# Kernel optimization log

Hardware: AMD Instinct MI355X
Metric: run time of the kernel (lower is better)

## Reference

```python
import jax, jax.numpy as jnp
import numpy as np

NMS_KS = 15
TOP_K = 2048
GAUSS_KS = 7
GAUSS_SIGMA = 1.0
LOSS_LAMBDA = 1.0


def setup_inputs() -> dict:
    key = jax.random.key(0)
    k1, k2, k3 = jax.random.split(key, 3)
    B, H, W = 16, 1024, 1024
    score1 = jax.random.uniform(k1, (B, 1, H, W), dtype=jnp.float32)
    w_score2 = jax.random.uniform(k2, (B, 1, H, W), dtype=jnp.float32)
    w_vis_mask2 = jax.random.randint(k3, (B, 1, H, W), 0, 2) > 0
    return {"score1": score1, "w_score2": w_score2, "w_vis_mask2": w_vis_mask2}


def _nms(score, ks):
    # keep only local maxima within a ks x ks window (stride 1, 'same' padding)
    pooled = jax.lax.reduce_window(score, -jnp.inf, jax.lax.max,
                                   (1, 1, ks, ks), (1, 1, 1, 1), 'SAME')
    return jnp.where(score == pooled, score, jnp.zeros_like(score))


def _prepare_gt_score(score, nms_ks, k, mask):
    # NMS -> mask -> per-image top-k -> binary GT keypoint map
    s = _nms(score, nms_ks) * mask.astype(score.dtype)
    b = s.shape[0]
    flat = s.reshape(b, -1)                      # B x (H*W)
    _, idx = jax.lax.top_k(flat, k)              # B x k
    gt = jnp.zeros_like(flat).at[jnp.arange(b)[:, None], idx].set(1.0)
    return gt.reshape(s.shape)


def _gaussian_filter(x, ks, sigma):
    coords = jnp.arange(ks, dtype=jnp.float32) - (ks - 1) / 2.0
    g = jnp.exp(-(coords ** 2) / (2.0 * sigma ** 2))
    g = g / g.sum()
    k2d = jnp.outer(g, g)[None, None]
    pad = ks // 2
    return jax.lax.conv_general_dilated(
        x, k2d, (1, 1), [(pad, pad), (pad, pad)],
        dimension_numbers=('NCHW', 'OIHW', 'NCHW'))


def reference(score1, w_score2, w_vis_mask2):
    b = score1.shape[0]
    gt_score1 = jax.lax.stop_gradient(
        _prepare_gt_score(w_score2, NMS_KS, TOP_K, w_vis_mask2))
    gt_score1 = _gaussian_filter(gt_score1, GAUSS_KS, GAUSS_SIGMA)
    m = w_vis_mask2.astype(jnp.float32)
    loss = ((score1 - gt_score1) ** 2) * m       # masked elementwise MSE
    loss = loss.reshape(b, -1).sum(-1) / jnp.clip(m.reshape(b, -1).sum(-1), 1e-8)
    return LOSS_LAMBDA * loss.mean()
```

## Files before the change

kernel.cpp:

```cpp
#include <hip/hip_runtime.h>
#include <math.h>

#define BATCH 16
#define H 1024
#define W 1024
#define NTILES 8192
#define NBANDS (NTILES * 4)
#define CAP 4096
#define TOPK 2048
#define BCW 12

struct WS {
  float pt1[NBANDS];
  int   pmc[NBANDS];
  int   band_cnt[NBANDS];
  int   cand_count[BATCH];
  float corr_part[BATCH * 64];
  float band_val[NBANDS * BCW];
  int   band_idx[NBANDS * BCW];
  float ccand_val[BATCH * CAP];
  int   ccand_idx[BATCH * CAP];
};

__constant__ float GW[7] = {
  0.004433048175f, 0.054005582623f, 0.242036229376f, 0.399050279652f,
  0.242036229376f, 0.054005582623f, 0.004433048175f
};

__device__ __forceinline__ float4 max4(float4 a, float4 b) {
  float4 r;
  r.x = fmaxf(a.x, b.x); r.y = fmaxf(a.y, b.y);
  r.z = fmaxf(a.z, b.z); r.w = fmaxf(a.w, b.w);
  return r;
}

__global__ __launch_bounds__(256, 5) void k_nms(const float* __restrict__ score1,
                                                const float* __restrict__ score2,
                                                const int* __restrict__ mask,
                                                WS* __restrict__ ws) {
  __shared__ float4 halo[4][22][21];
  const int tid = threadIdx.x;
  const int w = tid >> 6, l = tid & 63;

  const int t = (blockIdx.x & 7) * (NTILES / 8) + (blockIdx.x >> 3);
  const int b  = t >> 9;
  const int tt = t & 511;
  const int ty0 = (tt >> 4) << 5;
  const int tx0 = (tt & 15) << 6;
  const int by0 = ty0 + (w << 3);
  const size_t ibase = (size_t)b * ((size_t)H * W);
  const float* s2 = score2 + ibase;

  const int rl = l >> 3;
  const int c8 = l & 7;
  const size_t pb = ibase + (size_t)(by0 + rl) * W + tx0 + (c8 << 3);
  const float4 s1a = *(const float4*)(score1 + pb);
  const float4 s1b = *(const float4*)(score1 + pb + 4);
  const int4  mka = *(const int4*)(mask + pb);
  const int4  mkb = *(const int4*)(mask + pb + 4);

  float4 st[7]; int sr[7], sc[7];
  #pragma unroll
  for (int k = 0; k < 7; k++) {
    const int slot = l + (k << 6);
    if (slot < 440) {
      const int r = slot / 20, c = slot - r * 20;
      sr[k] = r; sc[k] = c;
      const int gy = by0 - 7 + r, gx = tx0 - 8 + (c << 2);
      const bool ok = (gy >= 0) & (gy < H) & (gx >= 0) & (gx < W);
      const int gyc = min(max(gy, 0), H - 1);
      const int gxc = ok ? gx : 0;
      float4 v = *(const float4*)(s2 + (size_t)gyc * W + gxc);
      if (!ok) v = make_float4(-INFINITY, -INFINITY, -INFINITY, -INFINITY);
      st[k] = v;
    }
  }

  float t1 = 0.f; int mcnt = 0; unsigned int mbits = 0;
  {
    const float sc_[8] = {s1a.x, s1a.y, s1a.z, s1a.w, s1b.x, s1b.y, s1b.z, s1b.w};
    const int   mm[8] = {mka.x, mka.y, mka.z, mka.w, mkb.x, mkb.y, mkb.z, mkb.w};
    #pragma unroll
    for (int j = 0; j < 8; j++) {
      if (mm[j]) { t1 = fmaf(sc_[j], sc_[j], t1); mcnt++; mbits |= (1u << j); }
    }
  }

  #pragma unroll
  for (int k = 0; k < 7; k++) {
    const int slot = l + (k << 6);
    if (slot < 440) halo[w][sr[k]][sc[k]] = st[k];
  }
  __builtin_amdgcn_wave_barrier();
  asm volatile("s_waitcnt lgkmcnt(0)" ::: "memory");
  __builtin_amdgcn_sched_barrier(0);

  float4 vr0, vr1, vr2, vr3;
  int R0 = 0, cg = 0;
  if (l < 40) {
    const int r2 = l / 20;
    cg = l - r2 * 20;
    R0 = r2 << 2;
    float4 core = halo[w][R0 + 3][cg];
    #pragma unroll
    for (int k = 4; k <= 14; k++) core = max4(core, halo[w][R0 + k][cg]);
    const float4 h0 = halo[w][R0][cg], h1 = halo[w][R0 + 1][cg], h2 = halo[w][R0 + 2][cg];
    const float4 h15 = halo[w][R0 + 15][cg], h16 = halo[w][R0 + 16][cg], h17 = halo[w][R0 + 17][cg];
    const float4 p2 = h2, p1 = max4(h1, p2), p0 = max4(h0, p1);
    const float4 sf15 = h15, sf16 = max4(sf15, h16), sf17 = max4(sf16, h17);
    vr0 = max4(core, p0);
    vr1 = max4(max4(core, p1), sf15);
    vr2 = max4(max4(core, p2), sf16);
    vr3 = max4(core, sf17);
  }
  const float4 cva = halo[w][rl + 7][(c8 << 1) + 2];
  const float4 cvb = halo[w][rl + 7][(c8 << 1) + 3];
  __builtin_amdgcn_wave_barrier();
  asm volatile("s_waitcnt lgkmcnt(0)" ::: "memory");
  __builtin_amdgcn_sched_barrier(0);

  if (l < 40) {
    halo[w][R0 + 0][cg] = vr0;
    halo[w][R0 + 1][cg] = vr1;
    halo[w][R0 + 2][cg] = vr2;
    halo[w][R0 + 3][cg] = vr3;
  }
  __builtin_amdgcn_wave_barrier();
  asm volatile("s_waitcnt lgkmcnt(0)" ::: "memory");
  __builtin_amdgcn_sched_barrier(0);

  float r[24];
  #pragma unroll
  for (int g = 0; g < 6; g++) {
    float4 v = halo[w][rl][(c8 << 1) + g];
    r[4 * g + 0] = v.x; r[4 * g + 1] = v.y; r[4 * g + 2] = v.z; r[4 * g + 3] = v.w;
  }
  float core = r[8];
  #pragma unroll
  for (int k = 9; k <= 15; k++) core = fmaxf(core, r[k]);
  const float q7 = r[7];
  const float q6 = fmaxf(r[6], q7);
  const float q5 = fmaxf(r[5], q6);
  const float q4 = fmaxf(r[4], q5);
  const float q3 = fmaxf(r[3], q4);
  const float q2 = fmaxf(r[2], q3);
  const float q1 = fmaxf(r[1], q2);
  float sa[7];
  sa[0] = r[16];
  #pragma unroll
  for (int k = 1; k < 7; k++) sa[k] = fmaxf(sa[k - 1], r[16 + k]);
  float pooled[8];
  pooled[0] = fmaxf(core, q1);
  pooled[1] = fmaxf(fmaxf(core, q2), sa[0]);
  pooled[2] = fmaxf(fmaxf(core, q3), sa[1]);
  pooled[3] = fmaxf(fmaxf(core, q4), sa[2]);
  pooled[4] = fmaxf(fmaxf(core, q5), sa[3]);
  pooled[5] = fmaxf(fmaxf(core, q6), sa[4]);
  pooled[6] = fmaxf(fmaxf(core, q7), sa[5]);
  pooled[7] = fmaxf(core, sa[6]);

  const float cc[8] = {cva.x, cva.y, cva.z, cva.w, cvb.x, cvb.y, cvb.z, cvb.w};
  int cj = -1; float cv = 0.f;
  #pragma unroll
  for (int j = 0; j < 8; j++) {
    if (((mbits >> j) & 1u) && cj < 0) {
      const float s = cc[j];
      if (s == pooled[j] && s > 0.f) { cj = j; cv = s; }
    }
  }
  const int band = (t << 2) + w;
  const unsigned long long bal = __ballot(cj >= 0);
  if (cj >= 0) {
    const int pos = (int)__popcll(bal & ((1ull << l) - 1ull));
    if (pos < BCW) {
      ws->band_val[band * BCW + pos] = cv;
      ws->band_idx[band * BCW + pos] = (by0 + rl) * W + tx0 + (c8 << 3) + cj;
    }
  }
  #pragma unroll
  for (int off = 32; off > 0; off >>= 1) {
    t1 += __shfl_down(t1, off);
    mcnt += __shfl_down(mcnt, off);
  }
  if (l == 0) {
    int nc = (int)__popcll(bal); if (nc > BCW) nc = BCW;
    ws->band_cnt[band] = nc;
    ws->pt1[band] = t1;
    ws->pmc[band] = mcnt;
  }
}

__global__ __launch_bounds__(256) void k_compact(WS* __restrict__ ws) {
  const int b = blockIdx.x;
  const int tid = threadIdx.x;
  const int lane = tid & 63, w = tid >> 6;
  __shared__ int wt[4];

  const int base = b * 2048 + tid * 8;
  int c[8]; int csum = 0;
  #pragma unroll
  for (int u = 0; u < 8; u++) {
    int x = ws->band_cnt[base + u];
    if (x > BCW) x = BCW;
    c[u] = x; csum += x;
  }
  int v = csum;
  #pragma unroll
  for (int off = 1; off < 64; off <<= 1) {
    int u2 = __shfl_up(v, off);
    if (lane >= off) v += u2;
  }
  if (lane == 63) wt[w] = v;
  __syncthreads();
  int wo = 0;
  #pragma unroll
  for (int k = 0; k < 4; k++) if (k < w) wo += wt[k];
  const int excl = v - csum + wo;
  float* dv = ws->ccand_val + b * CAP;
  int*   di = ws->ccand_idx + b * CAP;
  if (tid == 255) {
    int tot = excl + csum;
    if (tot > CAP) tot = CAP;
    ws->cand_count[b] = tot;
    #pragma unroll
    for (int u = 0; u < 3; u++)
      if (tot + u < CAP) dv[tot + u] = 0.f;
  }
  int off = excl;
  #pragma unroll
  for (int u = 0; u < 8; u++) {
    const float* sv = ws->band_val + (size_t)(base + u) * BCW;
    const int*   si = ws->band_idx + (size_t)(base + u) * BCW;
    for (int j = 0; j < c[u]; j++) {
      if (off < CAP) { dv[off] = sv[j]; di[off] = si[j]; }
      off++;
    }
  }
}

__global__ __launch_bounds__(256, 4) void k_rankstamp(const float* __restrict__ score1,
                                                      const int* __restrict__ mask,
                                                      WS* __restrict__ ws) {
  const int blk = (blockIdx.x & 7) * 128 + (blockIdx.x >> 3);
  const int b = blk >> 6;
  const int slice = blk & 63;
  int n = ws->cand_count[b]; if (n > CAP) n = CAP;
  const int i0 = slice << 6;
  if (i0 >= n) {
    if (threadIdx.x == 0) ws->corr_part[b * 64 + slice] = 0.f;
    return;
  }
  __shared__ __align__(16) float sval[CAP];
  __shared__ __align__(16) int   sidx[CAP];
  __shared__ int   s_prank[4][64];
  __shared__ int   s_keys[64];
  __shared__ int   s_nk;
  __shared__ float cred[4];
  const int tid = threadIdx.x;
  const int w = tid >> 6, l = tid & 63;
  const int nf4 = (n + 3) >> 2;

  const float4* gv = (const float4*)(ws->ccand_val + b * CAP);
  const int4*   gi = (const int4*)(ws->ccand_idx + b * CAP);
  for (int j = tid; j < nf4; j += 256) {
    ((float4*)sval)[j] = gv[j];
    ((int4*)sidx)[j]   = gi[j];
  }
  __syncthreads();

  const float vi = sval[i0 + l];
  const int   xi = sidx[i0 + l];
  const int q = (nf4 + 3) >> 2;
  int lo = w * q; if (lo > nf4) lo = nf4;
  int hi = lo + q; if (hi > nf4) hi = nf4;
  int rank = 0;
  int j = lo;
  for (; j + 4 <= hi; j += 4) {
    #pragma unroll
    for (int u = 0; u < 4; u++) {
      const float4 vv = ((const float4*)sval)[j + u];
      const int4  iv = ((const int4*)sidx)[j + u];
      rank += (vv.x > vi) + (vv.y > vi) + (vv.z > vi) + (vv.w > vi);
      rank += (vv.x == vi && iv.x < xi);
      rank += (vv.y == vi && iv.y < xi);
      rank += (vv.z == vi && iv.z < xi);
      rank += (vv.w == vi && iv.w < xi);
    }
  }
  for (; j < hi; j++) {
    const float4 vv = ((const float4*)sval)[j];
    const int4  iv = ((const int4*)sidx)[j];
    rank += (vv.x > vi) + (vv.y > vi) + (vv.z > vi) + (vv.w > vi);
    rank += (vv.x == vi && iv.x < xi);
    rank += (vv.y == vi && iv.y < xi);
    rank += (vv.z == vi && iv.z < xi);
    rank += (vv.w == vi && iv.w < xi);
  }
  s_prank[w][l] = rank;
  __syncthreads();

  if (tid < 64) {
    const int rtot = s_prank[0][tid] + s_prank[1][tid] + s_prank[2][tid] + s_prank[3][tid];
    const bool sel = (i0 + tid < n) && (rtot < TOPK);
    const unsigned long long bal = __ballot(sel);
    if (sel) {
      const int pos = __popcll(bal & ((1ull << tid) - 1ull));
      s_keys[pos] = sidx[i0 + tid];
    }
    if (tid == 0) s_nk = (int)__popcll(bal);
  }
  __syncthreads();
  const int nk = s_nk;

  float contrib = 0.f;
  const int sub = tid & 7;
  const size_t ib2 = (size_t)b * ((size_t)H * W);
  #pragma unroll
  for (int rnd = 0; rnd < 2; rnd++) {
    const int k = (tid >> 3) + (rnd << 5);
    if (k < nk && sub < 7) {
      const int ck = s_keys[k];
      const int cy = ck >> 10, cx = ck & 1023;
      const int py = cy + sub - 3;
      const float wy = GW[sub] * ((py >= 0 && py < H) ? 1.f : 0.f);
      const int pyc = min(max(py, 0), H - 1);
      const float* s1r = score1 + ib2 + (size_t)pyc * W;
      const int*   mr  = mask   + ib2 + (size_t)pyc * W;
      #pragma unroll
      for (int dx = -3; dx <= 3; dx++) {
        const int px = cx + dx;
        const float wv = wy * GW[dx + 3] * ((px >= 0 && px < W) ? 1.f : 0.f);
        const int pxc = min(max(px, 0), W - 1);
        const float mf = (mr[pxc] != 0) ? 1.f : 0.f;
        contrib += mf * wv * (wv - 2.f * s1r[pxc]);
      }
    }
  }
  #pragma unroll
  for (int off2 = 32; off2 > 0; off2 >>= 1) contrib += __shfl_down(contrib, off2);
  if (l == 0) cred[w] = contrib;
  __syncthreads();
  if (tid == 0)
    ws->corr_part[b * 64 + slice] = (cred[0] + cred[1]) + (cred[2] + cred[3]);
}

__global__ __launch_bounds__(1024) void k_final(WS* __restrict__ ws, float* __restrict__ out) {
  const int tid = threadIdx.x;
  const int b = tid >> 6, l = tid & 63;
  __shared__ double sD[BATCH];

  double tsum = 0.0; long long msum = 0;
  const float4* pv = (const float4*)(ws->pt1 + b * 2048);
  const int4*   pm = (const int4*)(ws->pmc + b * 2048);
  #pragma unroll
  for (int k = 0; k < 8; k++) {
    const float4 f = pv[l + (k << 6)];
    const int4   m = pm[l + (k << 6)];
    tsum += (double)f.x + (double)f.y + (double)f.z + (double)f.w;
    msum += (long long)(m.x + m.y + m.z + m.w);
  }
  double csum = (double)ws->corr_part[b * 64 + l];
  #pragma unroll
  for (int off = 32; off > 0; off >>= 1) {
    tsum += __shfl_down(tsum, off);
    msum += __shfl_down(msum, off);
    csum += __shfl_down(csum, off);
  }
  if (l == 0) {
    double denom = (double)msum;
    if (denom < 1e-8) denom = 1e-8;
    sD[b] = (tsum + csum) / denom;
  }
  __syncthreads();
  if (tid == 0) {
    double acc = 0.0;
    #pragma unroll
    for (int k = 0; k < BATCH; k++) acc += sD[k];
    out[0] = (float)(acc / BATCH);
  }
}

extern "C" void kernel_launch(void* const* d_in, const int* in_sizes, int n_in,
                              void* d_out, int out_size, void* d_ws, size_t ws_size,
                              hipStream_t stream) {
  const float* score1 = (const float*)d_in[0];
  const float* score2 = (const float*)d_in[1];
  const int*   mask   = (const int*)d_in[2];
  float* out = (float*)d_out;
  WS* ws = (WS*)d_ws;

  k_nms<<<NTILES, 256, 0, stream>>>(score1, score2, mask, ws);
  k_compact<<<BATCH, 256, 0, stream>>>(ws);
  k_rankstamp<<<BATCH * 64, 256, 0, stream>>>(score1, mask, ws);
  k_final<<<1, 1024, 0, stream>>>(ws, out);
}
```

Before: 85.65 us.

## Process full 32-row tile per wave to share vertical halo across bands

Each wave now owns a whole 32x64 tile and walks its four 8-row bands in sequence, using a single 46-row shared halo instead of four separate 22-row halos. This removes the redundant 14-row vertical halo reloads between adjacent bands and reduces global score2 traffic. The second half of the halo is loaded while the first band is computed. In exchange the kernel holds more registers and LDS per wave, runs 128-thread blocks with lower occupancy, and each wave's work is serialized.

```diff
diff --git a/kernel.cpp b/kernel.cpp
--- a/kernel.cpp
+++ b/kernel.cpp
@@ -6,9 +6,16 @@
 #define W 1024
 #define NTILES 8192
 #define NBANDS (NTILES * 4)
+#define NBLK 4096
 #define CAP 4096
 #define TOPK 2048
 #define BCW 12
+
+#define SYNC_WAVE() do { \
+  __builtin_amdgcn_wave_barrier(); \
+  asm volatile("s_waitcnt lgkmcnt(0)" ::: "memory"); \
+  __builtin_amdgcn_sched_barrier(0); \
+} while (0)
 
 struct WS {
   float pt1[NBANDS];
@@ -34,160 +41,192 @@
   return r;
 }
 
-__global__ __launch_bounds__(256, 5) void k_nms(const float* __restrict__ score1,
+__global__ __launch_bounds__(128, 2) void k_nms(const float* __restrict__ score1,
                                                 const float* __restrict__ score2,
                                                 const int* __restrict__ mask,
                                                 WS* __restrict__ ws) {
-  __shared__ float4 halo[4][22][21];
+  __shared__ float4 halo[2][46][21];
   const int tid = threadIdx.x;
   const int w = tid >> 6, l = tid & 63;
 
-  const int t = (blockIdx.x & 7) * (NTILES / 8) + (blockIdx.x >> 3);
+  const int blk = (blockIdx.x & 7) * (NBLK / 8) + (blockIdx.x >> 3);
+  const int t = (blk << 1) + w;
   const int b  = t >> 9;
   const int tt = t & 511;
   const int ty0 = (tt >> 4) << 5;
   const int tx0 = (tt & 15) << 6;
-  const int by0 = ty0 + (w << 3);
   const size_t ibase = (size_t)b * ((size_t)H * W);
   const float* s2 = score2 + ibase;
-
   const int rl = l >> 3;
   const int c8 = l & 7;
-  const size_t pb = ibase + (size_t)(by0 + rl) * W + tx0 + (c8 << 3);
-  const float4 s1a = *(const float4*)(score1 + pb);
-  const float4 s1b = *(const float4*)(score1 + pb + 4);
-  const int4  mka = *(const int4*)(mask + pb);
-  const int4  mkb = *(const int4*)(mask + pb + 4);
-
-  float4 st[7]; int sr[7], sc[7];
+
+  float4 s1a[4], s1b[4]; int4 mka[4], mkb[4];
+  #pragma unroll
+  for (int k = 0; k < 4; k++) {
+    const size_t pb = ibase + (size_t)(ty0 + (k << 3) + rl) * W + tx0 + (c8 << 3);
+    s1a[k] = *(const float4*)(score1 + pb);
+    s1b[k] = *(const float4*)(score1 + pb + 4);
+    mka[k] = *(const int4*)(mask + pb);
+    mkb[k] = *(const int4*)(mask + pb + 4);
+  }
+
+  float4 stA[7]; int rA[7], cA[7];
   #pragma unroll
   for (int k = 0; k < 7; k++) {
     const int slot = l + (k << 6);
     if (slot < 440) {
       const int r = slot / 20, c = slot - r * 20;
-      sr[k] = r; sc[k] = c;
-      const int gy = by0 - 7 + r, gx = tx0 - 8 + (c << 2);
+      rA[k] = r; cA[k] = c;
+      const int gy = ty0 - 7 + r, gx = tx0 - 8 + (c << 2);
       const bool ok = (gy >= 0) & (gy < H) & (gx >= 0) & (gx < W);
       const int gyc = min(max(gy, 0), H - 1);
       const int gxc = ok ? gx : 0;
       float4 v = *(const float4*)(s2 + (size_t)gyc * W + gxc);
       if (!ok) v = make_float4(-INFINITY, -INFINITY, -INFINITY, -INFINITY);
-      st[k] = v;
-    }
-  }
-
-  float t1 = 0.f; int mcnt = 0; unsigned int mbits = 0;
-  {
-    const float sc_[8] = {s1a.x, s1a.y, s1a.z, s1a.w, s1b.x, s1b.y, s1b.z, s1b.w};
-    const int   mm[8] = {mka.x, mka.y, mka.z, mka.w, mkb.x, mkb.y, mkb.z, mkb.w};
+      stA[k] = v;
+    }
+  }
+
+  float t1[4]; int mcnt[4]; unsigned int mbits[4];
+  #pragma unroll
+  for (int k = 0; k < 4; k++) {
+    t1[k] = 0.f; mcnt[k] = 0; mbits[k] = 0;
+    const float sc_[8] = {s1a[k].x, s1a[k].y, s1a[k].z, s1a[k].w,
+                          s1b[k].x, s1b[k].y, s1b[k].z, s1b[k].w};
+    const int   mm[8] = {mka[k].x, mka[k].y, mka[k].z, mka[k].w,
+                         mkb[k].x, mkb[k].y, mkb[k].z, mkb[k].w};
     #pragma unroll
     for (int j = 0; j < 8; j++) {
-      if (mm[j]) { t1 = fmaf(sc_[j], sc_[j], t1); mcnt++; mbits |= (1u << j); }
+      if (mm[j]) { t1[k] = fmaf(sc_[j], sc_[j], t1[k]); mcnt[k]++; mbits[k] |= (1u << j); }
+    }
+  }
+
+  float4 stB[8]; int rB[8], cB[8];
+  #pragma unroll
+  for (int k = 0; k < 8; k++) {
+    const int slot = 440 + l + (k << 6);
+    if (slot < 920) {
+      const int r = slot / 20, c = slot - r * 20;
+      rB[k] = r; cB[k] = c;
+      const int gy = ty0 - 7 + r, gx = tx0 - 8 + (c << 2);
+      const bool ok = (gy >= 0) & (gy < H) & (gx >= 0) & (gx < W);
+      const int gyc = min(max(gy, 0), H - 1);
+      const int gxc = ok ? gx : 0;
+      float4 v = *(const float4*)(s2 + (size_t)gyc * W + gxc);
+      if (!ok) v = make_float4(-INFINITY, -INFINITY, -INFINITY, -INFINITY);
+      stB[k] = v;
     }
   }
 
   #pragma unroll
   for (int k = 0; k < 7; k++) {
-    const int slot = l + (k << 6);
-    if (slot < 440) halo[w][sr[k]][sc[k]] = st[k];
-  }
-  __builtin_amdgcn_wave_barrier();
-  asm volatile("s_waitcnt lgkmcnt(0)" ::: "memory");
-  __builtin_amdgcn_sched_barrier(0);
-
-  float4 vr0, vr1, vr2, vr3;
-  int R0 = 0, cg = 0;
-  if (l < 40) {
-    const int r2 = l / 20;
-    cg = l - r2 * 20;
-    R0 = r2 << 2;
-    float4 core = halo[w][R0 + 3][cg];
-    #pragma unroll
-    for (int k = 4; k <= 14; k++) core = max4(core, halo[w][R0 + k][cg]);
-    const float4 h0 = halo[w][R0][cg], h1 = halo[w][R0 + 1][cg], h2 = halo[w][R0 + 2][cg];
-    const float4 h15 = halo[w][R0 + 15][cg], h16 = halo[w][R0 + 16][cg], h17 = halo[w][R0 + 17][cg];
-    const float4 p2 = h2, p1 = max4(h1, p2), p0 = max4(h0, p1);
-    const float4 sf15 = h15, sf16 = max4(sf15, h16), sf17 = max4(sf16, h17);
-    vr0 = max4(core, p0);
-    vr1 = max4(max4(core, p1), sf15);
-    vr2 = max4(max4(core, p2), sf16);
-    vr3 = max4(core, sf17);
-  }
-  const float4 cva = halo[w][rl + 7][(c8 << 1) + 2];
-  const float4 cvb = halo[w][rl + 7][(c8 << 1) + 3];
-  __builtin_amdgcn_wave_barrier();
-  asm volatile("s_waitcnt lgkmcnt(0)" ::: "memory");
-  __builtin_amdgcn_sched_barrier(0);
-
-  if (l < 40) {
-    halo[w][R0 + 0][cg] = vr0;
-    halo[w][R0 + 1][cg] = vr1;
-    halo[w][R0 + 2][cg] = vr2;
-    halo[w][R0 + 3][cg] = vr3;
-  }
-  __builtin_amdgcn_wave_barrier();
-  asm volatile("s_waitcnt lgkmcnt(0)" ::: "memory");
-  __builtin_amdgcn_sched_barrier(0);
-
-  float r[24];
-  #pragma unroll
-  for (int g = 0; g < 6; g++) {
-    float4 v = halo[w][rl][(c8 << 1) + g];
-    r[4 * g + 0] = v.x; r[4 * g + 1] = v.y; r[4 * g + 2] = v.z; r[4 * g + 3] = v.w;
-  }
-  float core = r[8];
-  #pragma unroll
-  for (int k = 9; k <= 15; k++) core = fmaxf(core, r[k]);
-  const float q7 = r[7];
-  const float q6 = fmaxf(r[6], q7);
-  const float q5 = fmaxf(r[5], q6);
-  const float q4 = fmaxf(r[4], q5);
-  const float q3 = fmaxf(r[3], q4);
-  const float q2 = fmaxf(r[2], q3);
-  const float q1 = fmaxf(r[1], q2);
-  float sa[7];
-  sa[0] = r[16];
-  #pragma unroll
-  for (int k = 1; k < 7; k++) sa[k] = fmaxf(sa[k - 1], r[16 + k]);
-  float pooled[8];
-  pooled[0] = fmaxf(core, q1);
-  pooled[1] = fmaxf(fmaxf(core, q2), sa[0]);
-  pooled[2] = fmaxf(fmaxf(core, q3), sa[1]);
-  pooled[3] = fmaxf(fmaxf(core, q4), sa[2]);
-  pooled[4] = fmaxf(fmaxf(core, q5), sa[3]);
-  pooled[5] = fmaxf(fmaxf(core, q6), sa[4]);
-  pooled[6] = fmaxf(fmaxf(core, q7), sa[5]);
-  pooled[7] = fmaxf(core, sa[6]);
-
-  const float cc[8] = {cva.x, cva.y, cva.z, cva.w, cvb.x, cvb.y, cvb.z, cvb.w};
-  int cj = -1; float cv = 0.f;
-  #pragma unroll
-  for (int j = 0; j < 8; j++) {
-    if (((mbits >> j) & 1u) && cj < 0) {
-      const float s = cc[j];
-      if (s == pooled[j] && s > 0.f) { cj = j; cv = s; }
-    }
-  }
-  const int band = (t << 2) + w;
-  const unsigned long long bal = __ballot(cj >= 0);
-  if (cj >= 0) {
-    const int pos = (int)__popcll(bal & ((1ull << l) - 1ull));
-    if (pos < BCW) {
-      ws->band_val[band * BCW + pos] = cv;
-      ws->band_idx[band * BCW + pos] = (by0 + rl) * W + tx0 + (c8 << 3) + cj;
-    }
-  }
-  #pragma unroll
-  for (int off = 32; off > 0; off >>= 1) {
-    t1 += __shfl_down(t1, off);
-    mcnt += __shfl_down(mcnt, off);
-  }
-  if (l == 0) {
-    int nc = (int)__popcll(bal); if (nc > BCW) nc = BCW;
-    ws->band_cnt[band] = nc;
-    ws->pt1[band] = t1;
-    ws->pmc[band] = mcnt;
-  }
+    if (l + (k << 6) < 440) halo[w][rA[k]][cA[k]] = stA[k];
+  }
+  SYNC_WAVE();
+
+  auto band_body = [&](int k) {
+    const int s0 = k << 3;
+    float4 vr0, vr1, vr2, vr3;
+    int R0 = 0, cg = 0;
+    if (l < 40) {
+      const int r2 = l / 20;
+      cg = l - r2 * 20;
+      R0 = s0 + (r2 << 2);
+      float4 core = halo[w][R0 + 3][cg];
+      #pragma unroll
+      for (int k2 = 4; k2 <= 14; k2++) core = max4(core, halo[w][R0 + k2][cg]);
+      const float4 h0 = halo[w][R0][cg], h1 = halo[w][R0 + 1][cg], h2 = halo[w][R0 + 2][cg];
+      const float4 h15 = halo[w][R0 + 15][cg], h16 = halo[w][R0 + 16][cg], h17 = halo[w][R0 + 17][cg];
+      const float4 p2 = h2, p1 = max4(h1, p2), p0 = max4(h0, p1);
+      const float4 sf15 = h15, sf16 = max4(sf15, h16), sf17 = max4(sf16, h17);
+      vr0 = max4(core, p0);
+      vr1 = max4(max4(core, p1), sf15);
+      vr2 = max4(max4(core, p2), sf16);
+      vr3 = max4(core, sf17);
+    }
+    const float4 cva = halo[w][s0 + rl + 7][(c8 << 1) + 2];
+    const float4 cvb = halo[w][s0 + rl + 7][(c8 << 1) + 3];
+    SYNC_WAVE();
+    if (l < 40) {
+      halo[w][R0 + 0][cg] = vr0;
+      halo[w][R0 + 1][cg] = vr1;
+      halo[w][R0 + 2][cg] = vr2;
+      halo[w][R0 + 3][cg] = vr3;
+    }
+    SYNC_WAVE();
+    float r[24];
+    #pragma unroll
+    for (int g = 0; g < 6; g++) {
+      float4 v = halo[w][s0 + rl][(c8 << 1) + g];
+      r[4 * g + 0] = v.x; r[4 * g + 1] = v.y; r[4 * g + 2] = v.z; r[4 * g + 3] = v.w;
+    }
+    float core = r[8];
+    #pragma unroll
+    for (int k2 = 9; k2 <= 15; k2++) core = fmaxf(core, r[k2]);
+    const float q7 = r[7];
+    const float q6 = fmaxf(r[6], q7);
+    const float q5 = fmaxf(r[5], q6);
+    const float q4 = fmaxf(r[4], q5);
+    const float q3 = fmaxf(r[3], q4);
+    const float q2 = fmaxf(r[2], q3);
+    const float q1 = fmaxf(r[1], q2);
+    float sa[7];
+    sa[0] = r[16];
+    #pragma unroll
+    for (int k2 = 1; k2 < 7; k2++) sa[k2] = fmaxf(sa[k2 - 1], r[16 + k2]);
+    float pooled[8];
+    pooled[0] = fmaxf(core, q1);
+    pooled[1] = fmaxf(fmaxf(core, q2), sa[0]);
+    pooled[2] = fmaxf(fmaxf(core, q3), sa[1]);
+    pooled[3] = fmaxf(fmaxf(core, q4), sa[2]);
+    pooled[4] = fmaxf(fmaxf(core, q5), sa[3]);
+    pooled[5] = fmaxf(fmaxf(core, q6), sa[4]);
+    pooled[6] = fmaxf(fmaxf(core, q7), sa[5]);
+    pooled[7] = fmaxf(core, sa[6]);
+
+    const float cc[8] = {cva.x, cva.y, cva.z, cva.w, cvb.x, cvb.y, cvb.z, cvb.w};
+    int cj = -1; float cv = 0.f;
+    #pragma unroll
+    for (int j = 0; j < 8; j++) {
+      if (((mbits[k] >> j) & 1u) && cj < 0) {
+        const float s = cc[j];
+        if (s == pooled[j] && s > 0.f) { cj = j; cv = s; }
+      }
+    }
+    const int band = (t << 2) + k;
+    const unsigned long long bal = __ballot(cj >= 0);
+    if (cj >= 0) {
+      const int pos = (int)__popcll(bal & ((1ull << l) - 1ull));
+      if (pos < BCW) {
+        ws->band_val[band * BCW + pos] = cv;
+        ws->band_idx[band * BCW + pos] = (ty0 + s0 + rl) * W + tx0 + (c8 << 3) + cj;
+      }
+    }
+    float rt1 = t1[k]; int rmc = mcnt[k];
+    #pragma unroll
+    for (int off = 32; off > 0; off >>= 1) {
+      rt1 += __shfl_down(rt1, off);
+      rmc += __shfl_down(rmc, off);
+    }
+    if (l == 0) {
+      int nc = (int)__popcll(bal); if (nc > BCW) nc = BCW;
+      ws->band_cnt[band] = nc;
+      ws->pt1[band] = rt1;
+      ws->pmc[band] = rmc;
+    }
+  };
+
+  band_body(0);
+
+  #pragma unroll
+  for (int k = 0; k < 8; k++) {
+    if (440 + l + (k << 6) < 920) halo[w][rB[k]][cB[k]] = stB[k];
+  }
+  SYNC_WAVE();
+
+  band_body(1);
+  band_body(2);
+  band_body(3);
 }
 
 __global__ __launch_bounds__(256) void k_compact(WS* __restrict__ ws) {
@@ -389,7 +428,7 @@
   float* out = (float*)d_out;
   WS* ws = (WS*)d_ws;
 
-  k_nms<<<NTILES, 256, 0, stream>>>(score1, score2, mask, ws);
+  k_nms<<<NBLK, 128, 0, stream>>>(score1, score2, mask, ws);
   k_compact<<<BATCH, 256, 0, stream>>>(ws);
   k_rankstamp<<<BATCH * 64, 256, 0, stream>>>(score1, mask, ws);
   k_final<<<1, 1024, 0, stream>>>(ws, out);
```

Result: slower. 95.43 us (+11.4%).
